# Kernel tuning notes

Hardware: AMD Instinct MI355X
Metric: run time of the kernel (lower is better)

## Reference

```python
import jax, jax.numpy as jnp
import numpy as np

N = 3072        # nodes
F_IN = 512      # input_dim
F_OUT = 256     # output_dim
ORDER = 2       # Cayley polynomial order
JACOBI = 3      # Jacobi fixed-point iterations per order


def setup_inputs() -> dict:
    key = jax.random.key(0)
    k1, k2, k3, k4, k5 = jax.random.split(key, 5)
    # normalized-adjacency-like matrix: row sums ~1 so h*Laplacian is well scaled
    adj = jax.random.uniform(k1, (N, N), dtype=jnp.float32) * (2.0 / N)
    x = jax.random.normal(k2, (N, F_IN), dtype=jnp.float32)
    h = jnp.float32(1.0)  # spectral zoom parameter
    w0 = jax.random.normal(k3, (F_IN, F_OUT), dtype=jnp.float32) * 0.05
    wr = jax.random.normal(k4, (ORDER, F_IN, F_OUT), dtype=jnp.float32) * 0.05
    wi = jax.random.normal(k5, (ORDER, F_IN, F_OUT), dtype=jnp.float32) * 0.05
    return {"x": x, "adj": adj, "h": h, "w0": w0, "wr": wr, "wi": wi}


def _cayley_forward(x, adj, h, w0, wr, wi):
    c64 = jnp.complex64
    j1 = jnp.asarray(1j, dtype=c64)
    n = adj.shape[0]
    I = jnp.eye(n, dtype=jnp.float32)
    # h * Laplacian, L = I - A_norm  (complex64, as in the TF code)
    hL = (h * (I - adj)).astype(c64)
    # Jacobi diagonal: rowsum(hL) + i  (constant across iterations)
    diag_inv = 1.0 / (jnp.sum(hL, axis=1) + j1)  # [n]

    # support[0] = I  ->  real part of I @ (x @ w0) is just x @ w0
    out = x @ w0  # [n, F_OUT] float32

    xc = x.astype(c64)
    csum = jnp.zeros((n, w0.shape[1]), dtype=c64)
    prev = I.astype(c64)
    for j in range(ORDER):
        # rhs of the linear system: x_j = hL @ prev - i*prev
        xj = hL @ prev - j1 * prev
        # Jacobi iterations: y <- y + D^{-1} (x_j - (hL @ y + i*y))
        y = xj
        for _ in range(JACOBI):
            y = y + diag_inv[:, None] * (xj - (hL @ y + j1 * y))
        W = jax.lax.complex(wr[j], wi[j])          # [F_IN, F_OUT] complex64
        csum = csum + y @ (xc @ W)                  # support_j @ pre_sup
        prev = y
    out = out + 2.0 * jnp.real(csum).astype(jnp.float32)
    return jax.nn.relu(out)


def reference(x, adj, h, w0, wr, wi):
    return _cayley_forward(x, adj, h, w0, wr, wi)
```

## Files before the change

### kernel.cpp

```cpp
#include <hip/hip_runtime.h>
#include <hip/hip_bf16.h>

#define NN 3072
#define FIN 512
#define FOUT 256

typedef __attribute__((ext_vector_type(8))) short short8;
typedef __attribute__((ext_vector_type(4))) float f32x4;

__device__ __forceinline__ short f2bf(float f) {
  union { float f; unsigned u; } v; v.f = f;
  unsigned r = v.u + 0x7fffu + ((v.u >> 16) & 1u);
  return (short)(r >> 16);
}

__device__ __forceinline__ void glds16(const short* g, short* l) {
  __builtin_amdgcn_global_load_lds(
      (const __attribute__((address_space(1))) unsigned*)g,
      (__attribute__((address_space(3))) unsigned*)l, 16, 0, 0);
}

template<int N> __device__ __forceinline__ void wait_vm() {
  if constexpr (N == 0)      asm volatile("s_waitcnt vmcnt(0)" ::: "memory");
  else if constexpr (N == 5) asm volatile("s_waitcnt vmcnt(5)" ::: "memory");
  else                       asm volatile("s_waitcnt vmcnt(10)" ::: "memory");
}


__global__ __launch_bounds__(256) void prep_adj(const float* __restrict__ adj,
    short* __restrict__ adjbf, float2* __restrict__ dinv, const float* __restrict__ hptr)
{
  int m = blockIdx.x;
  int tid = threadIdx.x;
  const float4* row = (const float4*)(adj + (size_t)m * NN);
  short4* obf = (short4*)(adjbf + (size_t)m * NN);
  float sum = 0.f;
#pragma unroll
  for (int i = 0; i < NN / 4 / 256; ++i) {
    int idx = i * 256 + tid;
    float4 v = row[idx];
    sum += (v.x + v.y) + (v.z + v.w);
    obf[idx] = make_short4(f2bf(v.x), f2bf(v.y), f2bf(v.z), f2bf(v.w));
  }
#pragma unroll
  for (int off = 32; off > 0; off >>= 1) sum += __shfl_down(sum, off, 64);
  __shared__ float red[4];
  if ((tid & 63) == 0) red[tid >> 6] = sum;
  __syncthreads();
  if (tid == 0) {
    float s = red[0] + red[1] + red[2] + red[3];
    float h = hptr[0];
    float r = h * (1.f - s);
    float den = r * r + 1.f;
    dinv[m] = make_float2(r / den, -1.f / den);
  }
}

__global__ __launch_bounds__(256) void prep_x(const float* __restrict__ x, short* __restrict__ xbf) {
  int idx = blockIdx.x * 256 + threadIdx.x;
  float4 v = ((const float4*)x)[idx];
  ((short4*)xbf)[idx] = make_short4(f2bf(v.x), f2bf(v.y), f2bf(v.z), f2bf(v.w));
}

__global__ __launch_bounds__(256) void prep_w(const float* __restrict__ w0,
    const float* __restrict__ wr, const float* __restrict__ wi, short* __restrict__ wpack)
{
  int idx = blockIdx.x * 256 + threadIdx.x;
  int f = idx & 511;
  int i = idx >> 9;
  float v;
  if (i < 1024) {
    int j = (i < 512) ? 1 : 0;
    int local = i & 511;
    int c = local >> 1;
    const float* src = (local & 1) ? wi : wr;
    v = src[((size_t)j * FIN + f) * FOUT + c];
  } else {
    v = w0[(size_t)f * FOUT + (i - 1024)];
  }
  wpack[idx] = f2bf(v);
}

template<int MODE, int KTOT>
__global__ __launch_bounds__(256, 2) void gemm_t(
    const short* __restrict__ Apan, int lda,
    const short* __restrict__ Badj, int ldb,
    const float* __restrict__ Vin,
    const float* __restrict__ Yin,
    float* __restrict__ Fout,
    short* __restrict__ Bout,
    const float2* __restrict__ dinv,
    const float* __restrict__ hptr)
{
  constexpr int BK = 64;
  constexpr int BM = 64;
  constexpr int BN = 96;
  constexpr int NT = KTOT / BK;
  constexpr int MR = 2;
  constexpr int AL = 2;
  constexpr int BL = 3;
  constexpr int LPW = AL + BL;

  __shared__ short As[2][BM * BK];
  __shared__ short Bs[2][BN * BK];

  const int tid  = threadIdx.x;
  const int lane = tid & 63;
  const int w    = tid >> 6;
  const int l15  = lane & 15;
  const int wrow = w >> 1, wcol = w & 1;

  const int i0 = blockIdx.y * BM;
  const int j0 = blockIdx.x * BN;

  const int srow = lane >> 3;
  const int scol = ((lane & 7) ^ srow) * 8;

  const short* aSrc = Apan + (size_t)i0 * lda;
  const short* bSrc = Badj + (size_t)j0 * ldb;

  auto STAGE = [&](int t) {
    const int k0 = t * BK;
    short* at = As[t & 1];
    short* bt = Bs[t & 1];
#pragma unroll
    for (int li = 0; li < AL; ++li) {
      int rb = (w + li * 4) * 8;
      glds16(aSrc + (size_t)(rb + srow) * lda + k0 + scol, at + rb * BK);
    }
#pragma unroll
    for (int li = 0; li < BL; ++li) {
      int rb = (w + li * 4) * 8;
      glds16(bSrc + (size_t)(rb + srow) * ldb + k0 + scol, bt + rb * BK);
    }
  };

  f32x4 acc[MR][3];
#pragma unroll
  for (int a = 0; a < MR; a++)
#pragma unroll
    for (int b = 0; b < 3; b++) acc[a][b] = (f32x4){0.f, 0.f, 0.f, 0.f};

  STAGE(0);
  STAGE(1);

  for (int t = 0; t < NT; ++t) {
    if (t < NT - 1) wait_vm<LPW>(); else wait_vm<0>();
    __builtin_amdgcn_s_barrier();
    asm volatile("" ::: "memory");

    const short* at = As[t & 1];
    const short* bt = Bs[t & 1];
#pragma unroll
    for (int kk = 0; kk < 2; ++kk) {
      const int cb = kk * 4 + (lane >> 4);
      short8 af[MR], bfr[3];
#pragma unroll
      for (int a = 0; a < MR; ++a) {
        int ra = wrow * 32 + a * 16 + l15;
        int c = cb ^ (ra & 7);
        af[a] = *(const short8*)(at + ra * BK + c * 8);
      }
#pragma unroll
      for (int b = 0; b < 3; ++b) {
        int rb = wcol * 48 + b * 16 + l15;
        int c = cb ^ (rb & 7);
        bfr[b] = *(const short8*)(bt + rb * BK + c * 8);
      }
#pragma unroll
      for (int a = 0; a < MR; ++a)
#pragma unroll
        for (int b = 0; b < 3; ++b)
          acc[a][b] = __builtin_amdgcn_mfma_f32_16x16x32_bf16(af[a], bfr[b], acc[a][b], 0, 0, 0);
    }

    asm volatile("" ::: "memory");
    __builtin_amdgcn_s_barrier();
    asm volatile("" ::: "memory");
    if (t + 2 < NT) STAGE(t + 2);
  }

  const float hv = hptr[0];
  const int ibase = i0 + wrow * 32 + ((lane >> 4) << 2);
#pragma unroll
  for (int a = 0; a < MR; ++a) {
    const int ia = ibase + a * 16;
#pragma unroll
    for (int b = 0; b < 3; ++b) {
      const int jb = j0 + wcol * 48 + b * 16 + l15;
      f32x4 c = acc[a][b];
      if (MODE == 0) {
#pragma unroll
        for (int q = 0; q < 4; ++q) {
          size_t off = (size_t)(ia + q) * NN + jb;
          Fout[off] = c[q];
          if (ia + q < 1024) Bout[off] = f2bf(c[q]);
        }
      } else if (MODE == 1) {
#pragma unroll
        for (int p = 0; p < 4; p += 2) {
          size_t offr = (size_t)(ia + p) * NN + jb;
          size_t offi = offr + NN;
          float vr = Vin[offr], vi = Vin[offi];
          float outr = hv * (vr - c[p])     + vi;
          float outi = hv * (vi - c[p + 1]) - vr;
          Fout[offr] = outr; Fout[offi] = outi;
          Bout[offr] = f2bf(outr); Bout[offi] = f2bf(outi);
        }
      } else {
#pragma unroll
        for (int p = 0; p < 4; p += 2) {
          size_t offr = (size_t)(ia + p) * NN + jb;
          size_t offi = offr + NN;
          float2 dv = dinv[jb];
          float vr = Vin[offr], vi = Vin[offi];
          float yr = Yin[offr], yi = Yin[offi];
          float tr_ = hv * (yr - c[p])     - yi;
          float ti_ = hv * (yi - c[p + 1]) + yr;
          float er = vr - tr_, ei = vi - ti_;
          float nyr = yr + dv.x * er - dv.y * ei;
          float nyi = yi + dv.x * ei + dv.y * er;
          Fout[offr] = nyr; Fout[offi] = nyi;
          Bout[offr] = f2bf(nyr); Bout[offi] = f2bf(nyi);
        }
      }
    }
  }
}

__global__ __launch_bounds__(256) void final_out(
    const float* __restrict__ Vbuf,
    const float* __restrict__ ybuf,
    float* __restrict__ out)
{
  __shared__ float t[64][65];
  int n0 = blockIdx.x * 64;
  int c0 = blockIdx.y * 64;
  int lane = threadIdx.x & 63;
  int wv = threadIdx.x >> 6;
#pragma unroll
  for (int s = 0; s < 16; s++) {
    int c = c0 + wv + s * 4;
    float o0 = Vbuf[(size_t)(1024 + c) * NN + n0 + lane];
    float u  = ybuf[(size_t)(2 * c) * NN + n0 + lane];
    float sv = ybuf[(size_t)(512 + 2 * c) * NN + n0 + lane];
    float v = o0 + 2.f * (u + sv);
    t[lane][wv + s * 4] = v > 0.f ? v : 0.f;
  }
  __syncthreads();
#pragma unroll
  for (int s = 0; s < 16; s++) {
    int nl = wv + s * 4;
    out[(size_t)(n0 + nl) * FOUT + c0 + lane] = t[nl][lane];
  }
}

extern "C" void kernel_launch(void* const* d_in, const int* in_sizes, int n_in,
                              void* d_out, int out_size, void* d_ws, size_t ws_size,
                              hipStream_t stream) {
  const float* x   = (const float*)d_in[0];
  const float* adj = (const float*)d_in[1];
  const float* h   = (const float*)d_in[2];
  const float* w0  = (const float*)d_in[3];
  const float* wr  = (const float*)d_in[4];
  const float* wi  = (const float*)d_in[5];
  float* out = (float*)d_out;

  char* ws = (char*)d_ws;
  size_t off = 0;
  auto alloc = [&](size_t bytes) {
    char* p = ws + off;
    off += (bytes + 255) & ~(size_t)255;
    return p;
  };
  short*  adjbf = (short*)alloc((size_t)NN * NN * 2);
  short*  xbf   = (short*)alloc((size_t)NN * FIN * 2);
  short*  wpack = (short*)alloc((size_t)1280 * FIN * 2);
  float2* dinv  = (float2*)alloc((size_t)NN * sizeof(float2));
  float*  Vbuf  = (float*)alloc((size_t)1280 * NN * 4);
  float*  ybuf  = (float*)alloc((size_t)1024 * NN * 4);
  short*  b0    = (short*)alloc((size_t)1024 * NN * 2);
  short*  b1    = (short*)alloc((size_t)1024 * NN * 2);

  prep_adj<<<NN, 256, 0, stream>>>(adj, adjbf, dinv, h);
  prep_x<<<(NN * FIN / 4) / 256, 256, 0, stream>>>(x, xbf);
  prep_w<<<(1280 * FIN) / 256, 256, 0, stream>>>(w0, wr, wi, wpack);

  gemm_t<0, FIN><<<dim3(32, 20), 256, 0, stream>>>(
      wpack, FIN, xbf, FIN, nullptr, nullptr, Vbuf, b0, dinv, h);
  gemm_t<1, NN><<<dim3(32, 16), 256, 0, stream>>>(
      b0, NN, adjbf, NN, Vbuf, nullptr, Vbuf, b1, dinv, h);
  gemm_t<2, NN><<<dim3(32, 16), 256, 0, stream>>>(
      b1, NN, adjbf, NN, Vbuf, Vbuf, ybuf, b0, dinv, h);
  gemm_t<2, NN><<<dim3(32, 16), 256, 0, stream>>>(
      b0, NN, adjbf, NN, Vbuf, ybuf, ybuf, b1, dinv, h);
  gemm_t<2, NN><<<dim3(32, 16), 256, 0, stream>>>(
      b1, NN, adjbf, NN, Vbuf, ybuf, ybuf, b0, dinv, h);
  gemm_t<1, NN><<<dim3(32, 8), 256, 0, stream>>>(
      b0, NN, adjbf, NN, ybuf, nullptr, Vbuf, b1, dinv, h);
  gemm_t<2, NN><<<dim3(32, 8), 256, 0, stream>>>(
      b1, NN, adjbf, NN, Vbuf, Vbuf, ybuf, b0, dinv, h);
  gemm_t<2, NN><<<dim3(32, 8), 256, 0, stream>>>(
      b0, NN, adjbf, NN, Vbuf, ybuf, ybuf, b1, dinv, h);
  gemm_t<2, NN><<<dim3(32, 8), 256, 0, stream>>>(
      b1, NN, adjbf, NN, Vbuf, ybuf, ybuf, b0, dinv, h);

  final_out<<<dim3(48, 4), 256, 0, stream>>>(Vbuf, ybuf, out);
}
```

Before: 376.2 us.

## Shrink GEMM tiles to 64x64, remap blocks per XCD, raise MFMA priority

Changes the GEMM tile from 64x96 to 64x64, which raises the block count, and raises launch bounds to 4 blocks per CU for more occupancy. Blocks are remapped from a 1D grid so that the blocks sharing an adjacency column panel land on the same XCD, aiming for better L2 reuse of the B operand. MFMA sections are wrapped in s_setprio to favour math issue. Smaller tiles lower the arithmetic intensity per block and add more redundant loads of A panels.

```diff
diff --git a/kernel.cpp b/kernel.cpp
--- a/kernel.cpp
+++ b/kernel.cpp
@@ -21,9 +21,8 @@
 }
 
 template<int N> __device__ __forceinline__ void wait_vm() {
-  if constexpr (N == 0)      asm volatile("s_waitcnt vmcnt(0)" ::: "memory");
-  else if constexpr (N == 5) asm volatile("s_waitcnt vmcnt(5)" ::: "memory");
-  else                       asm volatile("s_waitcnt vmcnt(10)" ::: "memory");
+  if constexpr (N == 0) asm volatile("s_waitcnt vmcnt(0)" ::: "memory");
+  else                  asm volatile("s_waitcnt vmcnt(4)" ::: "memory");
 }
 
 
@@ -81,8 +80,8 @@
   wpack[idx] = f2bf(v);
 }
 
-template<int MODE, int KTOT>
-__global__ __launch_bounds__(256, 2) void gemm_t(
+template<int MODE, int KTOT, int ITILES>
+__global__ __launch_bounds__(256, 4) void gemm_t(
     const short* __restrict__ Apan, int lda,
     const short* __restrict__ Badj, int ldb,
     const float* __restrict__ Vin,
@@ -93,16 +92,10 @@
     const float* __restrict__ hptr)
 {
   constexpr int BK = 64;
-  constexpr int BM = 64;
-  constexpr int BN = 96;
   constexpr int NT = KTOT / BK;
-  constexpr int MR = 2;
-  constexpr int AL = 2;
-  constexpr int BL = 3;
-  constexpr int LPW = AL + BL;
-
-  __shared__ short As[2][BM * BK];
-  __shared__ short Bs[2][BN * BK];
+
+  __shared__ short As[2][64 * BK];
+  __shared__ short Bs[2][64 * BK];
 
   const int tid  = threadIdx.x;
   const int lane = tid & 63;
@@ -110,8 +103,14 @@
   const int l15  = lane & 15;
   const int wrow = w >> 1, wcol = w & 1;
 
-  const int i0 = blockIdx.y * BM;
-  const int j0 = blockIdx.x * BN;
+  const int bid = blockIdx.x;
+  const int xcd = bid & 7;
+  const int s   = bid >> 3;
+  const int jt  = xcd * 6 + s / ITILES;
+  const int it  = s % ITILES;
+
+  const int i0 = it * 64;
+  const int j0 = jt * 64;
 
   const int srow = lane >> 3;
   const int scol = ((lane & 7) ^ srow) * 8;
@@ -124,28 +123,28 @@
     short* at = As[t & 1];
     short* bt = Bs[t & 1];
 #pragma unroll
-    for (int li = 0; li < AL; ++li) {
-      int rb = (w + li * 4) * 8;
+    for (int li = 0; li < 2; ++li) {
+      int rb = (w * 2 + li) * 8;
       glds16(aSrc + (size_t)(rb + srow) * lda + k0 + scol, at + rb * BK);
     }
 #pragma unroll
-    for (int li = 0; li < BL; ++li) {
-      int rb = (w + li * 4) * 8;
+    for (int li = 0; li < 2; ++li) {
+      int rb = (w * 2 + li) * 8;
       glds16(bSrc + (size_t)(rb + srow) * ldb + k0 + scol, bt + rb * BK);
     }
   };
 
-  f32x4 acc[MR][3];
-#pragma unroll
-  for (int a = 0; a < MR; a++)
-#pragma unroll
-    for (int b = 0; b < 3; b++) acc[a][b] = (f32x4){0.f, 0.f, 0.f, 0.f};
+  f32x4 acc[2][2];
+#pragma unroll
+  for (int a = 0; a < 2; a++)
+#pragma unroll
+    for (int b = 0; b < 2; b++) acc[a][b] = (f32x4){0.f, 0.f, 0.f, 0.f};
 
   STAGE(0);
   STAGE(1);
 
   for (int t = 0; t < NT; ++t) {
-    if (t < NT - 1) wait_vm<LPW>(); else wait_vm<0>();
+    if (t < NT - 1) wait_vm<4>(); else wait_vm<0>();
     __builtin_amdgcn_s_barrier();
     asm volatile("" ::: "memory");
 
@@ -154,24 +153,26 @@
 #pragma unroll
     for (int kk = 0; kk < 2; ++kk) {
       const int cb = kk * 4 + (lane >> 4);
-      short8 af[MR], bfr[3];
-#pragma unroll
-      for (int a = 0; a < MR; ++a) {
+      short8 af[2], bfr[2];
+#pragma unroll
+      for (int a = 0; a < 2; ++a) {
         int ra = wrow * 32 + a * 16 + l15;
         int c = cb ^ (ra & 7);
         af[a] = *(const short8*)(at + ra * BK + c * 8);
       }
 #pragma unroll
-      for (int b = 0; b < 3; ++b) {
-        int rb = wcol * 48 + b * 16 + l15;
+      for (int b = 0; b < 2; ++b) {
+        int rb = wcol * 32 + b * 16 + l15;
         int c = cb ^ (rb & 7);
         bfr[b] = *(const short8*)(bt + rb * BK + c * 8);
       }
-#pragma unroll
-      for (int a = 0; a < MR; ++a)
-#pragma unroll
-        for (int b = 0; b < 3; ++b)
+      __builtin_amdgcn_s_setprio(1);
+#pragma unroll
+      for (int a = 0; a < 2; ++a)
+#pragma unroll
+        for (int b = 0; b < 2; ++b)
           acc[a][b] = __builtin_amdgcn_mfma_f32_16x16x32_bf16(af[a], bfr[b], acc[a][b], 0, 0, 0);
+      __builtin_amdgcn_s_setprio(0);
     }
 
     asm volatile("" ::: "memory");
@@ -183,11 +184,11 @@
   const float hv = hptr[0];
   const int ibase = i0 + wrow * 32 + ((lane >> 4) << 2);
 #pragma unroll
-  for (int a = 0; a < MR; ++a) {
+  for (int a = 0; a < 2; ++a) {
     const int ia = ibase + a * 16;
 #pragma unroll
-    for (int b = 0; b < 3; ++b) {
-      const int jb = j0 + wcol * 48 + b * 16 + l15;
+    for (int b = 0; b < 2; ++b) {
+      const int jb = j0 + wcol * 32 + b * 16 + l15;
       f32x4 c = acc[a][b];
       if (MODE == 0) {
 #pragma unroll
@@ -286,23 +287,23 @@
   prep_x<<<(NN * FIN / 4) / 256, 256, 0, stream>>>(x, xbf);
   prep_w<<<(1280 * FIN) / 256, 256, 0, stream>>>(w0, wr, wi, wpack);
 
-  gemm_t<0, FIN><<<dim3(32, 20), 256, 0, stream>>>(
+  gemm_t<0, FIN, 20><<<dim3(48 * 20), 256, 0, stream>>>(
       wpack, FIN, xbf, FIN, nullptr, nullptr, Vbuf, b0, dinv, h);
-  gemm_t<1, NN><<<dim3(32, 16), 256, 0, stream>>>(
+  gemm_t<1, NN, 16><<<dim3(48 * 16), 256, 0, stream>>>(
       b0, NN, adjbf, NN, Vbuf, nullptr, Vbuf, b1, dinv, h);
-  gemm_t<2, NN><<<dim3(32, 16), 256, 0, stream>>>(
+  gemm_t<2, NN, 16><<<dim3(48 * 16), 256, 0, stream>>>(
       b1, NN, adjbf, NN, Vbuf, Vbuf, ybuf, b0, dinv, h);
-  gemm_t<2, NN><<<dim3(32, 16), 256, 0, stream>>>(
+  gemm_t<2, NN, 16><<<dim3(48 * 16), 256, 0, stream>>>(
       b0, NN, adjbf, NN, Vbuf, ybuf, ybuf, b1, dinv, h);
-  gemm_t<2, NN><<<dim3(32, 16), 256, 0, stream>>>(
+  gemm_t<2, NN, 16><<<dim3(48 * 16), 256, 0, stream>>>(
       b1, NN, adjbf, NN, Vbuf, ybuf, ybuf, b0, dinv, h);
-  gemm_t<1, NN><<<dim3(32, 8), 256, 0, stream>>>(
+  gemm_t<1, NN, 8><<<dim3(48 * 8), 256, 0, stream>>>(
       b0, NN, adjbf, NN, ybuf, nullptr, Vbuf, b1, dinv, h);
-  gemm_t<2, NN><<<dim3(32, 8), 256, 0, stream>>>(
+  gemm_t<2, NN, 8><<<dim3(48 * 8), 256, 0, stream>>>(
       b1, NN, adjbf, NN, Vbuf, Vbuf, ybuf, b0, dinv, h);
-  gemm_t<2, NN><<<dim3(32, 8), 256, 0, stream>>>(
+  gemm_t<2, NN, 8><<<dim3(48 * 8), 256, 0, stream>>>(
       b0, NN, adjbf, NN, Vbuf, ybuf, ybuf, b1, dinv, h);
-  gemm_t<2, NN><<<dim3(32, 8), 256, 0, stream>>>(
+  gemm_t<2, NN, 8><<<dim3(48 * 8), 256, 0, stream>>>(
       b1, NN, adjbf, NN, Vbuf, ybuf, ybuf, b0, dinv, h);
 
   final_out<<<dim3(48, 4), 256, 0, stream>>>(Vbuf, ybuf, out);
```

New measurement: 381.9 us. Within noise of the previous version (+1.5%).
